# Kernel optimization log

Hardware: AMD Instinct MI355X
Metric: run time of the kernel (lower is better)

Reference implementation:

```python
import jax, jax.numpy as jnp
import numpy as np

B, T, C = 4, 2048, 1024
T_PAST = 2048


def setup_inputs() -> dict:
    key = jax.random.key(0)
    ks = jax.random.split(key, 9)
    s = 1.0 / np.sqrt(C)
    return {
        "x": jax.random.normal(ks[0], (B, T, C), dtype=jnp.float32),
        "past_k": jax.random.normal(ks[1], (B, T_PAST, C), dtype=jnp.float32),
        "past_v": jax.random.normal(ks[2], (B, T_PAST, C), dtype=jnp.float32),
        "Wq": jax.random.normal(ks[3], (C, C), dtype=jnp.float32) * s,
        "bq": jnp.zeros((C,), dtype=jnp.float32),
        "Wk": jax.random.normal(ks[4], (C, C), dtype=jnp.float32) * s,
        "bk": jnp.zeros((C,), dtype=jnp.float32),
        "Wv": jax.random.normal(ks[5], (C, C), dtype=jnp.float32) * s,
        "bv": jnp.zeros((C,), dtype=jnp.float32),
    }


def reference(x, past_k, past_v, Wq, bq, Wk, bk, Wv, bv):
    Bb, Tt, Cc = x.shape
    # nn.Linear: y = x @ W^T + b
    Q = jnp.einsum('btc,dc->btd', x, Wq) + bq
    K = jnp.einsum('btc,dc->btd', x, Wk) + bk
    V = jnp.einsum('btc,dc->btd', x, Wv) + bv
    K = jnp.concatenate([past_k, K], axis=1)
    V = jnp.concatenate([past_v, V], axis=1)
    T_total = K.shape[1]
    scores = jnp.einsum('btc,bsc->bts', Q, K) / jnp.sqrt(jnp.float32(Cc))
    # Faithful to torch.tril(ones(T, T_total)): allow j <= i (even across cache)
    mask = jnp.arange(T_total)[None, :] <= jnp.arange(Tt)[:, None]
    scores = jnp.where(mask[None, :, :], scores, -jnp.inf)
    weights = jax.nn.softmax(scores, axis=-1)
    out = jnp.einsum('bts,bsc->btc', weights, V)
    return (out, K, V)
```

## Files before the change

kernel.cpp:

```cpp
#include <hip/hip_runtime.h>


typedef __bf16 bf16x8 __attribute__((ext_vector_type(8)));
typedef float f32x4 __attribute__((ext_vector_type(4)));

#define BB   4
#define TQ   2048
#define CD   1024
#define TPAST 2048
#define TTOT 4096
#define MROWS (BB * TQ)
#define SSTRIDE ((size_t)TTOT * CD * 2)

__device__ __forceinline__ unsigned short f32_to_bf16u(float f) {
  unsigned int u = __float_as_uint(f);
  u += 0x7FFFu + ((u >> 16) & 1u);
  return (unsigned short)(u >> 16);
}
__device__ __forceinline__ float bf16u_to_f32(unsigned short h) {
  unsigned int u = ((unsigned int)h) << 16;
  return __uint_as_float(u);
}
__device__ __forceinline__ unsigned int pack_bf16(float a, float b) {
  return (unsigned int)f32_to_bf16u(a) | ((unsigned int)f32_to_bf16u(b) << 16);
}

__device__ __forceinline__ void gload_lds16(const unsigned short* g,
                                            unsigned short* l) {
  __builtin_amdgcn_global_load_lds(
      (const __attribute__((address_space(1))) void*)g,
      (__attribute__((address_space(3))) void*)l, 16, 0, 0);
}

#define R0_END 2097152
#define R1_END 2359296
#define R2_END 2621440
#define R3_END 2883584
#define R4_END 4980736
__global__ __launch_bounds__(256) void cvt_all(
    const float* __restrict__ x, const float* __restrict__ wq,
    const float* __restrict__ wk, const float* __restrict__ wv,
    const float* __restrict__ pk,
    unsigned short* __restrict__ xb, unsigned short* __restrict__ wqb,
    unsigned short* __restrict__ wkb, unsigned short* __restrict__ wvb,
    unsigned short* __restrict__ kb) {
  int i = blockIdx.x * 256 + threadIdx.x;
  const float* src; unsigned short* dst; int off;
  if (i < R0_END)      { src = x;  dst = xb;  off = i; }
  else if (i < R1_END) { src = wq; dst = wqb; off = i - R0_END; }
  else if (i < R2_END) { src = wk; dst = wkb; off = i - R1_END; }
  else if (i < R3_END) { src = wv; dst = wvb; off = i - R2_END; }
  else                 { src = pk; dst = kb;  off = i - R3_END; }
  float4 f = ((const float4*)src)[off];
  uint2 o;
  o.x = pack_bf16(f.x, f.y);
  o.y = pack_bf16(f.z, f.w);
  ((uint2*)dst)[off] = o;
}

__global__ __launch_bounds__(256) void copy_past_kernel(
    const float* __restrict__ src, float* __restrict__ dst) {
  int i = blockIdx.x * 256 + threadIdx.x;
  int b = i >> 19;
  int rem = i & 524287;
  ((float4*)dst)[(size_t)b * 1048576 + rem] = ((const float4*)src)[i];
}

#define TP_PAD 134
__global__ __launch_bounds__(256) void v_copy_transpose(
    const float* __restrict__ pV, float* __restrict__ outV,
    unsigned short* __restrict__ VT) {
  __shared__ unsigned short T[32 * TP_PAD];
  const int s0 = blockIdx.x * 32, c0 = blockIdx.y * 128, b = blockIdx.z;
  const int tid = threadIdx.x;
  const int s = tid >> 3, i8 = tid & 7;
  const float* src = &pV[(size_t)(b * TPAST + s0 + s) * CD + c0];
  float* dst = &outV[(size_t)b * (TTOT * CD) + (size_t)(s0 + s) * CD + c0];
#pragma unroll
  for (int k = 0; k < 4; ++k) {
    int c = k * 32 + i8 * 4;
    float4 f = *(const float4*)&src[c];
    *(float4*)&dst[c] = f;
    *(unsigned int*)&T[s * TP_PAD + c]     = pack_bf16(f.x, f.y);
    *(unsigned int*)&T[s * TP_PAD + c + 2] = pack_bf16(f.z, f.w);
  }
  __syncthreads();
  const int c = tid >> 2, sq = tid & 3;
#pragma unroll
  for (int ii = 0; ii < 2; ++ii) {
    int cc = c + ii * 64;
    unsigned short tmp[8];
#pragma unroll
    for (int j = 0; j < 8; ++j) tmp[j] = T[(sq * 8 + j) * TP_PAD + cc];
    *(uint4*)&VT[(size_t)(b * CD + c0 + cc) * TPAST + s0 + sq * 8] = *(uint4*)tmp;
  }
}

__global__ __launch_bounds__(256) void proj_qkv(
    const unsigned short* __restrict__ A,
    const unsigned short* __restrict__ Wq_,
    const unsigned short* __restrict__ Wv_,
    const unsigned short* __restrict__ Wk_,
    const float* __restrict__ bq_, const float* __restrict__ bv_,
    const float* __restrict__ bk_,
    unsigned short* __restrict__ outQ,
    float* __restrict__ outV,
    float* __restrict__ outK) {
  __shared__ unsigned short sA[128 * 32];
  __shared__ unsigned short sB[128 * 32];
  const int tm = blockIdx.x * 128;
  const int which = blockIdx.y >> 3;
  const int tn = (blockIdx.y & 7) * 128;
  const unsigned short* W = (which == 0) ? Wq_ : (which == 1) ? Wv_ : Wk_;
  const float* bias = (which == 0) ? bq_ : (which == 1) ? bv_ : bk_;
  const int tid = threadIdx.x, lane = tid & 63, wv = tid >> 6;
  const int wr = wv >> 1, wc = wv & 1;
  const int gr = lane >> 2, gc = (lane & 3) * 8;
  const unsigned short* aSrc = &A[(size_t)(tm + wv * 32 + gr) * CD + gc];
  const unsigned short* bSrc = &W[(size_t)(tn + wv * 32 + gr) * CD + gc];
  unsigned short* aDst = &sA[wv * 32 * 32];
  unsigned short* bDst = &sB[wv * 32 * 32];
  f32x4 acc[4][4] = {};
  for (int k0 = 0; k0 < CD; k0 += 32) {
    gload_lds16(aSrc + k0, aDst);
    gload_lds16(aSrc + k0 + (size_t)16 * CD, aDst + 16 * 32);
    gload_lds16(bSrc + k0, bDst);
    gload_lds16(bSrc + k0 + (size_t)16 * CD, bDst + 16 * 32);
    __syncthreads();
    bf16x8 af[4], bg[4];
    const int koff = (lane >> 4) * 8;
#pragma unroll
    for (int i = 0; i < 4; ++i)
      af[i] = *(const bf16x8*)&sA[(wr * 64 + i * 16 + (lane & 15)) * 32 + koff];
#pragma unroll
    for (int i = 0; i < 4; ++i)
      bg[i] = *(const bf16x8*)&sB[(wc * 64 + i * 16 + (lane & 15)) * 32 + koff];
#pragma unroll
    for (int mi = 0; mi < 4; ++mi)
#pragma unroll
      for (int ni = 0; ni < 4; ++ni)
        acc[mi][ni] = __builtin_amdgcn_mfma_f32_16x16x32_bf16(
            af[mi], bg[ni], acc[mi][ni], 0, 0, 0);
    __syncthreads();
  }
  const int rsub = (lane >> 4) * 4, csub = lane & 15;
#pragma unroll
  for (int mi = 0; mi < 4; ++mi)
#pragma unroll
    for (int ni = 0; ni < 4; ++ni) {
      int gcn = tn + wc * 64 + ni * 16 + csub;
      float bvv = bias[gcn];
#pragma unroll
      for (int r = 0; r < 4; ++r) {
        int grw = tm + wr * 64 + mi * 16 + rsub + r;
        float v = acc[mi][ni][r] + bvv;
        if (which == 0) {
          outQ[(size_t)grw * CD + gcn] = f32_to_bf16u(v * 0.03125f);
        } else {
          int b = grw >> 11, t = grw & (TQ - 1);
          float* o = (which == 1) ? outV : outK;
          o[(size_t)b * (TTOT * CD) + (size_t)(TPAST + t) * CD + gcn] = v;
        }
      }
    }
}

__global__ __launch_bounds__(256) void score_gemm(
    const unsigned short* __restrict__ Q,
    const unsigned short* __restrict__ KB,
    unsigned short* __restrict__ S16) {
  const int t0 = blockIdx.x * 128, s0 = blockIdx.y * 128, b = blockIdx.z;
  if (s0 > t0 + 127) return;
  __shared__ unsigned short sA[128 * 32];
  __shared__ unsigned short sB[128 * 32];
  const int tid = threadIdx.x, lane = tid & 63, wv = tid >> 6;
  const int wr = wv >> 1, wc = wv & 1;
  const int gr = lane >> 2, gc = (lane & 3) * 8;
  const unsigned short* aSrc = &Q[(size_t)(b * TQ + t0 + wv * 32 + gr) * CD + gc];
  const unsigned short* bSrc = &KB[(size_t)(b * TPAST + s0 + wv * 32 + gr) * CD + gc];
  unsigned short* aDst = &sA[wv * 32 * 32];
  unsigned short* bDst = &sB[wv * 32 * 32];
  f32x4 acc[4][4] = {};
  for (int k0 = 0; k0 < CD; k0 += 32) {
    gload_lds16(aSrc + k0, aDst);
    gload_lds16(aSrc + k0 + (size_t)16 * CD, aDst + 16 * 32);
    gload_lds16(bSrc + k0, bDst);
    gload_lds16(bSrc + k0 + (size_t)16 * CD, bDst + 16 * 32);
    __syncthreads();
    bf16x8 af[4], bg[4];
    const int koff = (lane >> 4) * 8;
#pragma unroll
    for (int i = 0; i < 4; ++i)
      af[i] = *(const bf16x8*)&sA[(wr * 64 + i * 16 + (lane & 15)) * 32 + koff];
#pragma unroll
    for (int i = 0; i < 4; ++i)
      bg[i] = *(const bf16x8*)&sB[(wc * 64 + i * 16 + (lane & 15)) * 32 + koff];
#pragma unroll
    for (int mi = 0; mi < 4; ++mi)
#pragma unroll
      for (int ni = 0; ni < 4; ++ni)
        acc[mi][ni] = __builtin_amdgcn_mfma_f32_16x16x32_bf16(
            af[mi], bg[ni], acc[mi][ni], 0, 0, 0);
    __syncthreads();
  }
  const int rsub = (lane >> 4) * 4, csub = lane & 15;
#pragma unroll
  for (int mi = 0; mi < 4; ++mi)
#pragma unroll
    for (int ni = 0; ni < 4; ++ni) {
      int gs = s0 + wc * 64 + ni * 16 + csub;
#pragma unroll
      for (int r = 0; r < 4; ++r) {
        int gt = t0 + wr * 64 + mi * 16 + rsub + r;
        S16[(size_t)b * SSTRIDE + (size_t)gt * TPAST + gs] =
            f32_to_bf16u(acc[mi][ni][r]);
      }
    }
}

__global__ __launch_bounds__(256) void softmax_kernel(unsigned short* __restrict__ S16) {
  const int row = blockIdx.x;
  const int b = row >> 11, t = row & (TQ - 1);
  unsigned short* p = S16 + (size_t)b * SSTRIDE + (size_t)t * TPAST;
  const int tid = threadIdx.x, lane = tid & 63, wv = tid >> 6;
  __shared__ float red[8];
  const int base = tid * 8;
  uint4 raw = *(const uint4*)&p[base];
  const unsigned short* rw = (const unsigned short*)&raw;
  float v[8];
  float m = -3.0e38f;
#pragma unroll
  for (int i = 0; i < 8; ++i) {
    v[i] = (base + i <= t) ? bf16u_to_f32(rw[i]) : -3.0e38f;
    m = fmaxf(m, v[i]);
  }
#pragma unroll
  for (int off = 32; off >= 1; off >>= 1) m = fmaxf(m, __shfl_down(m, off));
  if (lane == 0) red[wv] = m;
  __syncthreads();
  if (tid == 0) red[4] = fmaxf(fmaxf(red[0], red[1]), fmaxf(red[2], red[3]));
  __syncthreads();
  const float rm = red[4];
  float e[8], s = 0.f;
#pragma unroll
  for (int i = 0; i < 8; ++i) {
    e[i] = (base + i <= t) ? __expf(v[i] - rm) : 0.f;
    s += e[i];
  }
#pragma unroll
  for (int off = 32; off >= 1; off >>= 1) s += __shfl_down(s, off);
  __syncthreads();
  if (lane == 0) red[wv] = s;
  __syncthreads();
  if (tid == 0) red[5] = red[0] + red[1] + red[2] + red[3];
  __syncthreads();
  const float inv = 1.f / red[5];
  unsigned short ob[8];
#pragma unroll
  for (int i = 0; i < 8; ++i) ob[i] = f32_to_bf16u(e[i] * inv);
  *(uint4*)&p[base] = *(uint4*)ob;
}

__global__ __launch_bounds__(256) void pv_gemm(
    const unsigned short* __restrict__ Pb,
    const unsigned short* __restrict__ VT,
    float* __restrict__ O) {
  const int t0 = blockIdx.x * 128, c0 = blockIdx.y * 128, b = blockIdx.z;
  __shared__ unsigned short sA[128 * 32];
  __shared__ unsigned short sB[128 * 32];
  const int tid = threadIdx.x, lane = tid & 63, wv = tid >> 6;
  const int wr = wv >> 1, wc = wv & 1;
  const int gr = lane >> 2, gc = (lane & 3) * 8;
  const unsigned short* aSrc =
      &Pb[(size_t)b * SSTRIDE + (size_t)(t0 + wv * 32 + gr) * TPAST + gc];
  const unsigned short* bSrc =
      &VT[(size_t)(b * CD + c0 + wv * 32 + gr) * TPAST + gc];
  unsigned short* aDst = &sA[wv * 32 * 32];
  unsigned short* bDst = &sB[wv * 32 * 32];
  f32x4 acc[4][4] = {};
  const int s_end = (t0 + 128 < TPAST) ? (t0 + 128) : TPAST;
  for (int s0 = 0; s0 < s_end; s0 += 32) {
    gload_lds16(aSrc + s0, aDst);
    gload_lds16(aSrc + s0 + (size_t)16 * TPAST, aDst + 16 * 32);
    gload_lds16(bSrc + s0, bDst);
    gload_lds16(bSrc + s0 + (size_t)16 * TPAST, bDst + 16 * 32);
    __syncthreads();
    bf16x8 af[4], bg[4];
    const int koff = (lane >> 4) * 8;
#pragma unroll
    for (int i = 0; i < 4; ++i)
      af[i] = *(const bf16x8*)&sA[(wr * 64 + i * 16 + (lane & 15)) * 32 + koff];
#pragma unroll
    for (int i = 0; i < 4; ++i)
      bg[i] = *(const bf16x8*)&sB[(wc * 64 + i * 16 + (lane & 15)) * 32 + koff];
#pragma unroll
    for (int mi = 0; mi < 4; ++mi)
#pragma unroll
      for (int ni = 0; ni < 4; ++ni)
        acc[mi][ni] = __builtin_amdgcn_mfma_f32_16x16x32_bf16(
            af[mi], bg[ni], acc[mi][ni], 0, 0, 0);
    __syncthreads();
  }
  const int rsub = (lane >> 4) * 4, csub = lane & 15;
#pragma unroll
  for (int mi = 0; mi < 4; ++mi)
#pragma unroll
    for (int ni = 0; ni < 4; ++ni) {
      int gcn = c0 + wc * 64 + ni * 16 + csub;
#pragma unroll
      for (int r = 0; r < 4; ++r) {
        int gt = t0 + wr * 64 + mi * 16 + rsub + r;
        O[(size_t)(b * TQ + gt) * CD + gcn] = acc[mi][ni][r];
      }
    }
}

extern "C" void kernel_launch(void* const* d_in, const int* in_sizes, int n_in,
                              void* d_out, int out_size, void* d_ws, size_t ws_size,
                              hipStream_t stream) {
  const float* x  = (const float*)d_in[0];
  const float* pk = (const float*)d_in[1];
  const float* pv = (const float*)d_in[2];
  const float* Wq = (const float*)d_in[3];
  const float* bq = (const float*)d_in[4];
  const float* Wk = (const float*)d_in[5];
  const float* bk = (const float*)d_in[6];
  const float* Wv = (const float*)d_in[7];
  const float* bv = (const float*)d_in[8];

  float* out  = (float*)d_out;
  float* outK = out + (size_t)BB * TQ * CD;
  float* outV = outK + (size_t)BB * TTOT * CD;
  unsigned short* S16 = (unsigned short*)outK;

  unsigned short* xb  = (unsigned short*)d_ws;
  unsigned short* wqb = xb + (size_t)MROWS * CD;
  unsigned short* wkb = wqb + (size_t)CD * CD;
  unsigned short* wvb = wkb + (size_t)CD * CD;
  unsigned short* qb  = wvb + (size_t)CD * CD;
  unsigned short* vtb = qb + (size_t)MROWS * CD;
  unsigned short* kb  = vtb + (size_t)BB * CD * TPAST;

  cvt_all<<<R4_END / 256, 256, 0, stream>>>(x, Wq, Wk, Wv, pk,
                                            xb, wqb, wkb, wvb, kb);
  v_copy_transpose<<<dim3(TPAST / 32, CD / 128, BB), 256, 0, stream>>>(pv, outV, vtb);
  proj_qkv<<<dim3(MROWS / 128, 24), 256, 0, stream>>>(
      xb, wqb, wvb, wkb, bq, bv, bk, qb, outV, outK);
  score_gemm<<<dim3(TQ / 128, TPAST / 128, BB), 256, 0, stream>>>(qb, kb, S16);
  softmax_kernel<<<BB * TQ, 256, 0, stream>>>(S16);
  pv_gemm<<<dim3(TQ / 128, CD / 128, BB), 256, 0, stream>>>(S16, vtb, out);
  copy_past_kernel<<<BB * TPAST * CD / 4 / 256, 256, 0, stream>>>(pk, outK);
}
```

Before: 240.4 us.

## Double-buffer LDS tiles in GEMMs and merge prep kernels into one launch

The projection, score and PV GEMMs now use two LDS buffers per operand: the global-to-LDS load for the next K-tile is issued before the MFMAs on the current tile, so load latency can overlap compute. The bf16 conversion kernel and the V copy/transpose kernel are merged into a single launch whose block index selects the role, removing one kernel launch and its tail. The cost is doubled LDS use per block, which may lower occupancy, plus a shared-memory array that the conversion blocks allocate but never use.

```diff
diff --git a/kernel.cpp b/kernel.cpp
--- a/kernel.cpp
+++ b/kernel.cpp
@@ -32,19 +32,50 @@
       (__attribute__((address_space(3))) void*)l, 16, 0, 0);
 }
 
+#define TP_PAD 134
+#define VCT_BLOCKS 2048
 #define R0_END 2097152
 #define R1_END 2359296
 #define R2_END 2621440
 #define R3_END 2883584
 #define R4_END 4980736
-__global__ __launch_bounds__(256) void cvt_all(
+__global__ __launch_bounds__(256) void prep(
     const float* __restrict__ x, const float* __restrict__ wq,
     const float* __restrict__ wk, const float* __restrict__ wv,
-    const float* __restrict__ pk,
+    const float* __restrict__ pk, const float* __restrict__ pV,
     unsigned short* __restrict__ xb, unsigned short* __restrict__ wqb,
     unsigned short* __restrict__ wkb, unsigned short* __restrict__ wvb,
-    unsigned short* __restrict__ kb) {
-  int i = blockIdx.x * 256 + threadIdx.x;
+    unsigned short* __restrict__ kb,
+    float* __restrict__ outV, unsigned short* __restrict__ VT) {
+  const int tid = threadIdx.x;
+  if (blockIdx.x < VCT_BLOCKS) {
+    __shared__ unsigned short T[32 * TP_PAD];
+    const int bid = blockIdx.x;
+    const int s0 = (bid & 63) * 32, c0 = ((bid >> 6) & 7) * 128, b = bid >> 9;
+    const int s = tid >> 3, i8 = tid & 7;
+    const float* src = &pV[(size_t)(b * TPAST + s0 + s) * CD + c0];
+    float* dst = &outV[(size_t)b * (TTOT * CD) + (size_t)(s0 + s) * CD + c0];
+#pragma unroll
+    for (int k = 0; k < 4; ++k) {
+      int c = k * 32 + i8 * 4;
+      float4 f = *(const float4*)&src[c];
+      *(float4*)&dst[c] = f;
+      *(unsigned int*)&T[s * TP_PAD + c]     = pack_bf16(f.x, f.y);
+      *(unsigned int*)&T[s * TP_PAD + c + 2] = pack_bf16(f.z, f.w);
+    }
+    __syncthreads();
+    const int c = tid >> 2, sq = tid & 3;
+#pragma unroll
+    for (int ii = 0; ii < 2; ++ii) {
+      int cc = c + ii * 64;
+      unsigned short tmp[8];
+#pragma unroll
+      for (int j = 0; j < 8; ++j) tmp[j] = T[(sq * 8 + j) * TP_PAD + cc];
+      *(uint4*)&VT[(size_t)(b * CD + c0 + cc) * TPAST + s0 + sq * 8] = *(uint4*)tmp;
+    }
+    return;
+  }
+  int i = (blockIdx.x - VCT_BLOCKS) * 256 + tid;
   const float* src; unsigned short* dst; int off;
   if (i < R0_END)      { src = x;  dst = xb;  off = i; }
   else if (i < R1_END) { src = wq; dst = wqb; off = i - R0_END; }
@@ -66,36 +97,6 @@
   ((float4*)dst)[(size_t)b * 1048576 + rem] = ((const float4*)src)[i];
 }
 
-#define TP_PAD 134
-__global__ __launch_bounds__(256) void v_copy_transpose(
-    const float* __restrict__ pV, float* __restrict__ outV,
-    unsigned short* __restrict__ VT) {
-  __shared__ unsigned short T[32 * TP_PAD];
-  const int s0 = blockIdx.x * 32, c0 = blockIdx.y * 128, b = blockIdx.z;
-  const int tid = threadIdx.x;
-  const int s = tid >> 3, i8 = tid & 7;
-  const float* src = &pV[(size_t)(b * TPAST + s0 + s) * CD + c0];
-  float* dst = &outV[(size_t)b * (TTOT * CD) + (size_t)(s0 + s) * CD + c0];
-#pragma unroll
-  for (int k = 0; k < 4; ++k) {
-    int c = k * 32 + i8 * 4;
-    float4 f = *(const float4*)&src[c];
-    *(float4*)&dst[c] = f;
-    *(unsigned int*)&T[s * TP_PAD + c]     = pack_bf16(f.x, f.y);
-    *(unsigned int*)&T[s * TP_PAD + c + 2] = pack_bf16(f.z, f.w);
-  }
-  __syncthreads();
-  const int c = tid >> 2, sq = tid & 3;
-#pragma unroll
-  for (int ii = 0; ii < 2; ++ii) {
-    int cc = c + ii * 64;
-    unsigned short tmp[8];
-#pragma unroll
-    for (int j = 0; j < 8; ++j) tmp[j] = T[(sq * 8 + j) * TP_PAD + cc];
-    *(uint4*)&VT[(size_t)(b * CD + c0 + cc) * TPAST + s0 + sq * 8] = *(uint4*)tmp;
-  }
-}
-
 __global__ __launch_bounds__(256) void proj_qkv(
     const unsigned short* __restrict__ A,
     const unsigned short* __restrict__ Wq_,
@@ -106,8 +107,8 @@
     unsigned short* __restrict__ outQ,
     float* __restrict__ outV,
     float* __restrict__ outK) {
-  __shared__ unsigned short sA[128 * 32];
-  __shared__ unsigned short sB[128 * 32];
+  __shared__ unsigned short sA[2][128 * 32];
+  __shared__ unsigned short sB[2][128 * 32];
   const int tm = blockIdx.x * 128;
   const int which = blockIdx.y >> 3;
   const int tn = (blockIdx.y & 7) * 128;
@@ -118,23 +119,31 @@
   const int gr = lane >> 2, gc = (lane & 3) * 8;
   const unsigned short* aSrc = &A[(size_t)(tm + wv * 32 + gr) * CD + gc];
   const unsigned short* bSrc = &W[(size_t)(tn + wv * 32 + gr) * CD + gc];
-  unsigned short* aDst = &sA[wv * 32 * 32];
-  unsigned short* bDst = &sB[wv * 32 * 32];
+  const int ldsOff = wv * 32 * 32;
   f32x4 acc[4][4] = {};
-  for (int k0 = 0; k0 < CD; k0 += 32) {
-    gload_lds16(aSrc + k0, aDst);
-    gload_lds16(aSrc + k0 + (size_t)16 * CD, aDst + 16 * 32);
-    gload_lds16(bSrc + k0, bDst);
-    gload_lds16(bSrc + k0 + (size_t)16 * CD, bDst + 16 * 32);
-    __syncthreads();
+  const int NT = CD / 32;
+  gload_lds16(aSrc, &sA[0][ldsOff]);
+  gload_lds16(aSrc + (size_t)16 * CD, &sA[0][ldsOff + 16 * 32]);
+  gload_lds16(bSrc, &sB[0][ldsOff]);
+  gload_lds16(bSrc + (size_t)16 * CD, &sB[0][ldsOff + 16 * 32]);
+  __syncthreads();
+  for (int t = 0; t < NT; ++t) {
+    const int cur = t & 1;
+    if (t + 1 < NT) {
+      const int k0 = (t + 1) * 32, nb = cur ^ 1;
+      gload_lds16(aSrc + k0, &sA[nb][ldsOff]);
+      gload_lds16(aSrc + k0 + (size_t)16 * CD, &sA[nb][ldsOff + 16 * 32]);
+      gload_lds16(bSrc + k0, &sB[nb][ldsOff]);
+      gload_lds16(bSrc + k0 + (size_t)16 * CD, &sB[nb][ldsOff + 16 * 32]);
+    }
     bf16x8 af[4], bg[4];
     const int koff = (lane >> 4) * 8;
 #pragma unroll
     for (int i = 0; i < 4; ++i)
-      af[i] = *(const bf16x8*)&sA[(wr * 64 + i * 16 + (lane & 15)) * 32 + koff];
-#pragma unroll
-    for (int i = 0; i < 4; ++i)
-      bg[i] = *(const bf16x8*)&sB[(wc * 64 + i * 16 + (lane & 15)) * 32 + koff];
+      af[i] = *(const bf16x8*)&sA[cur][(wr * 64 + i * 16 + (lane & 15)) * 32 + koff];
+#pragma unroll
+    for (int i = 0; i < 4; ++i)
+      bg[i] = *(const bf16x8*)&sB[cur][(wc * 64 + i * 16 + (lane & 15)) * 32 + koff];
 #pragma unroll
     for (int mi = 0; mi < 4; ++mi)
 #pragma unroll
@@ -171,30 +180,38 @@
     unsigned short* __restrict__ S16) {
   const int t0 = blockIdx.x * 128, s0 = blockIdx.y * 128, b = blockIdx.z;
   if (s0 > t0 + 127) return;
-  __shared__ unsigned short sA[128 * 32];
-  __shared__ unsigned short sB[128 * 32];
+  __shared__ unsigned short sA[2][128 * 32];
+  __shared__ unsigned short sB[2][128 * 32];
   const int tid = threadIdx.x, lane = tid & 63, wv = tid >> 6;
   const int wr = wv >> 1, wc = wv & 1;
   const int gr = lane >> 2, gc = (lane & 3) * 8;
   const unsigned short* aSrc = &Q[(size_t)(b * TQ + t0 + wv * 32 + gr) * CD + gc];
   const unsigned short* bSrc = &KB[(size_t)(b * TPAST + s0 + wv * 32 + gr) * CD + gc];
-  unsigned short* aDst = &sA[wv * 32 * 32];
-  unsigned short* bDst = &sB[wv * 32 * 32];
+  const int ldsOff = wv * 32 * 32;
   f32x4 acc[4][4] = {};
-  for (int k0 = 0; k0 < CD; k0 += 32) {
-    gload_lds16(aSrc + k0, aDst);
-    gload_lds16(aSrc + k0 + (size_t)16 * CD, aDst + 16 * 32);
-    gload_lds16(bSrc + k0, bDst);
-    gload_lds16(bSrc + k0 + (size_t)16 * CD, bDst + 16 * 32);
-    __syncthreads();
+  const int NT = CD / 32;
+  gload_lds16(aSrc, &sA[0][ldsOff]);
+  gload_lds16(aSrc + (size_t)16 * CD, &sA[0][ldsOff + 16 * 32]);
+  gload_lds16(bSrc, &sB[0][ldsOff]);
+  gload_lds16(bSrc + (size_t)16 * CD, &sB[0][ldsOff + 16 * 32]);
+  __syncthreads();
+  for (int t = 0; t < NT; ++t) {
+    const int cur = t & 1;
+    if (t + 1 < NT) {
+      const int k0 = (t + 1) * 32, nb = cur ^ 1;
+      gload_lds16(aSrc + k0, &sA[nb][ldsOff]);
+      gload_lds16(aSrc + k0 + (size_t)16 * CD, &sA[nb][ldsOff + 16 * 32]);
+      gload_lds16(bSrc + k0, &sB[nb][ldsOff]);
+      gload_lds16(bSrc + k0 + (size_t)16 * CD, &sB[nb][ldsOff + 16 * 32]);
+    }
     bf16x8 af[4], bg[4];
     const int koff = (lane >> 4) * 8;
 #pragma unroll
     for (int i = 0; i < 4; ++i)
-      af[i] = *(const bf16x8*)&sA[(wr * 64 + i * 16 + (lane & 15)) * 32 + koff];
-#pragma unroll
-    for (int i = 0; i < 4; ++i)
-      bg[i] = *(const bf16x8*)&sB[(wc * 64 + i * 16 + (lane & 15)) * 32 + koff];
+      af[i] = *(const bf16x8*)&sA[cur][(wr * 64 + i * 16 + (lane & 15)) * 32 + koff];
+#pragma unroll
+    for (int i = 0; i < 4; ++i)
+      bg[i] = *(const bf16x8*)&sB[cur][(wc * 64 + i * 16 + (lane & 15)) * 32 + koff];
 #pragma unroll
     for (int mi = 0; mi < 4; ++mi)
 #pragma unroll
@@ -266,8 +283,8 @@
     const unsigned short* __restrict__ VT,
     float* __restrict__ O) {
   const int t0 = blockIdx.x * 128, c0 = blockIdx.y * 128, b = blockIdx.z;
-  __shared__ unsigned short sA[128 * 32];
-  __shared__ unsigned short sB[128 * 32];
+  __shared__ unsigned short sA[2][128 * 32];
+  __shared__ unsigned short sB[2][128 * 32];
   const int tid = threadIdx.x, lane = tid & 63, wv = tid >> 6;
   const int wr = wv >> 1, wc = wv & 1;
   const int gr = lane >> 2, gc = (lane & 3) * 8;
@@ -275,24 +292,32 @@
       &Pb[(size_t)b * SSTRIDE + (size_t)(t0 + wv * 32 + gr) * TPAST + gc];
   const unsigned short* bSrc =
       &VT[(size_t)(b * CD + c0 + wv * 32 + gr) * TPAST + gc];
-  unsigned short* aDst = &sA[wv * 32 * 32];
-  unsigned short* bDst = &sB[wv * 32 * 32];
+  const int ldsOff = wv * 32 * 32;
   f32x4 acc[4][4] = {};
   const int s_end = (t0 + 128 < TPAST) ? (t0 + 128) : TPAST;
-  for (int s0 = 0; s0 < s_end; s0 += 32) {
-    gload_lds16(aSrc + s0, aDst);
-    gload_lds16(aSrc + s0 + (size_t)16 * TPAST, aDst + 16 * 32);
-    gload_lds16(bSrc + s0, bDst);
-    gload_lds16(bSrc + s0 + (size_t)16 * TPAST, bDst + 16 * 32);
-    __syncthreads();
+  const int NT = s_end / 32;
+  gload_lds16(aSrc, &sA[0][ldsOff]);
+  gload_lds16(aSrc + (size_t)16 * TPAST, &sA[0][ldsOff + 16 * 32]);
+  gload_lds16(bSrc, &sB[0][ldsOff]);
+  gload_lds16(bSrc + (size_t)16 * TPAST, &sB[0][ldsOff + 16 * 32]);
+  __syncthreads();
+  for (int t = 0; t < NT; ++t) {
+    const int cur = t & 1;
+    if (t + 1 < NT) {
+      const int s0 = (t + 1) * 32, nb = cur ^ 1;
+      gload_lds16(aSrc + s0, &sA[nb][ldsOff]);
+      gload_lds16(aSrc + s0 + (size_t)16 * TPAST, &sA[nb][ldsOff + 16 * 32]);
+      gload_lds16(bSrc + s0, &sB[nb][ldsOff]);
+      gload_lds16(bSrc + s0 + (size_t)16 * TPAST, &sB[nb][ldsOff + 16 * 32]);
+    }
     bf16x8 af[4], bg[4];
     const int koff = (lane >> 4) * 8;
 #pragma unroll
     for (int i = 0; i < 4; ++i)
-      af[i] = *(const bf16x8*)&sA[(wr * 64 + i * 16 + (lane & 15)) * 32 + koff];
-#pragma unroll
-    for (int i = 0; i < 4; ++i)
-      bg[i] = *(const bf16x8*)&sB[(wc * 64 + i * 16 + (lane & 15)) * 32 + koff];
+      af[i] = *(const bf16x8*)&sA[cur][(wr * 64 + i * 16 + (lane & 15)) * 32 + koff];
+#pragma unroll
+    for (int i = 0; i < 4; ++i)
+      bg[i] = *(const bf16x8*)&sB[cur][(wc * 64 + i * 16 + (lane & 15)) * 32 + koff];
 #pragma unroll
     for (int mi = 0; mi < 4; ++mi)
 #pragma unroll
@@ -341,9 +366,8 @@
   unsigned short* vtb = qb + (size_t)MROWS * CD;
   unsigned short* kb  = vtb + (size_t)BB * CD * TPAST;
 
-  cvt_all<<<R4_END / 256, 256, 0, stream>>>(x, Wq, Wk, Wv, pk,
-                                            xb, wqb, wkb, wvb, kb);
-  v_copy_transpose<<<dim3(TPAST / 32, CD / 128, BB), 256, 0, stream>>>(pv, outV, vtb);
+  prep<<<VCT_BLOCKS + R4_END / 256, 256, 0, stream>>>(
+      x, Wq, Wk, Wv, pk, pv, xb, wqb, wkb, wvb, kb, outV, vtb);
   proj_qkv<<<dim3(MROWS / 128, 24), 256, 0, stream>>>(
       xb, wqb, wvb, wkb, bq, bv, bk, qb, outV, outK);
   score_gemm<<<dim3(TQ / 128, TPAST / 128, BB), 256, 0, stream>>>(qb, kb, S16);
```

Result: no change. 238.2 us (-0.9%).
